# Performance work log

Measured on AMD Instinct MI355X. Metric: run time of the kernel, lower is better.

## Reference

```python
import jax, jax.numpy as jnp
import numpy as np

E = 1024
H = 16
D = E // H  # 64
S = 2048
B = 4


def setup_inputs() -> dict:
    key = jax.random.key(0)
    ks = jax.random.split(key, 9)
    scale = 1.0 / np.sqrt(E)
    inp = {"x": jax.random.normal(ks[0], (S, B, E), dtype=jnp.float32)}
    for i, name in enumerate(["q", "k", "v", "o"]):
        inp[f"W{name}"] = jax.random.uniform(ks[1 + 2 * i], (E, E), dtype=jnp.float32, minval=-scale, maxval=scale)
        inp[f"b{name}"] = jax.random.uniform(ks[2 + 2 * i], (E,), dtype=jnp.float32, minval=-scale, maxval=scale)
    return inp


def reference(x, Wq, bq, Wk, bk, Wv, bv, Wo, bo):
    s, b, e = x.shape
    # linear projections (torch Linear: x @ W.T + b), split into heads
    q = (x @ Wq.T + bq).reshape(s, b, H, D)
    k = (x @ Wk.T + bk).reshape(s, b, H, D)
    v = (x @ Wv.T + bv).reshape(s, b, H, D)
    # naive O(S^2) attention, scores: [S, B, H, S]
    scores = jnp.einsum('sbhd,tbhd->sbht', q, k) / np.sqrt(D).astype(np.float32)
    attn = jax.nn.softmax(scores, axis=3)
    # dropout p=0.0 (eval) -> identity
    out = jnp.einsum('sbht,tbhd->sbhd', attn, v).reshape(s, b, e)
    return out @ Wo.T + bo
```

## Files before the change

### kernel.cpp

```cpp
#include <hip/hip_runtime.h>
#include <hip/hip_bf16.h>

#define S_LEN 2048
#define BATCH 4
#define EMB   1024
#define NH    16
#define HD    64
#define NROW  8192

#define QSCALE 0.18033688011112043f

typedef __bf16 bf16x8 __attribute__((ext_vector_type(8)));
typedef float  f32x4  __attribute__((ext_vector_type(4)));

typedef __attribute__((address_space(3))) void lds_void;
typedef const __attribute__((address_space(1))) void gbl_void;
#define GLOAD_LDS16(g, l) __builtin_amdgcn_global_load_lds((gbl_void*)(g), (lds_void*)(l), 16, 0, 0)
#define MFMA16(a, b, c) __builtin_amdgcn_mfma_f32_16x16x32_bf16((a), (b), (c), 0, 0, 0)

#if __has_builtin(__builtin_amdgcn_exp2f)
#define EXP2(x) __builtin_amdgcn_exp2f(x)
#else
#define EXP2(x) __expf((x) * 0.6931471805599453f)
#endif

__global__ void cvt_all_kernel(const float* __restrict__ x,
                               const float* __restrict__ wq, const float* __restrict__ wk,
                               const float* __restrict__ wv, const float* __restrict__ wo,
                               __bf16* __restrict__ xb,
                               __bf16* __restrict__ qb, __bf16* __restrict__ kb,
                               __bf16* __restrict__ vb, __bf16* __restrict__ ob) {
    const int bid = blockIdx.x;
    const float* src;
    __bf16* dst;
    int i;
    if (bid < 8192) {
        src = x; dst = xb; i = bid * 256 + threadIdx.x;
    } else {
        const int w = (bid - 8192) >> 10;
        src = w == 0 ? wq : (w == 1 ? wk : (w == 2 ? wv : wo));
        dst = w == 0 ? qb : (w == 1 ? kb : (w == 2 ? vb : ob));
        i = ((bid - 8192) & 1023) * 256 + threadIdx.x;
    }
    float4 v = ((const float4*)src)[i];
    union { __bf16 h[4]; short4 s4; } u;
    u.h[0] = (__bf16)v.x; u.h[1] = (__bf16)v.y;
    u.h[2] = (__bf16)v.z; u.h[3] = (__bf16)v.w;
    ((short4*)dst)[i] = u.s4;
}

__global__ __launch_bounds__(256) void gemm_qkv_kernel(
    const __bf16* __restrict__ A,
    const __bf16* __restrict__ W0, const __bf16* __restrict__ W1,
    const __bf16* __restrict__ W2,
    const float* __restrict__ bi0, const float* __restrict__ bi1,
    const float* __restrict__ bi2,
    __bf16* __restrict__ Qo, __bf16* __restrict__ Ko, __bf16* __restrict__ Vo)
{
    __shared__ __align__(16) char SMEM[49152];
    __bf16* Asb = (__bf16*)SMEM;
    __bf16* Bsb = (__bf16*)(SMEM + 24576);

    const int flat = blockIdx.x;
    const int xcd = flat & 7, slot = flat >> 3;
    const int nB = slot >> 3;
    const int mB = (xcd << 3) | (slot & 7);
    const int which = nB >> 3;
    const __bf16* W = which == 0 ? W0 : (which == 1 ? W1 : W2);
    const float* bias = which == 0 ? bi0 : (which == 1 ? bi1 : bi2);
    __bf16* outb = which == 0 ? Qo : (which == 1 ? Ko : Vo);
    const int m0 = mB * 128;
    const int n0 = (nB & 7) * 128;

    const int lane = threadIdx.x & 63;
    const int wave = threadIdx.x >> 6;
    const int l15 = lane & 15;
    const int quad = lane >> 4;
    const int wm = (wave >> 1) * 64;
    const int wn = (wave & 1) * 64;

    const int c0 = wave * 128 + lane;
    const int c1 = c0 + 64;
    const int ar0 = c0 >> 2, ak0 = (((c0 & 3) ^ ((c0 >> 3) & 3))) * 8;
    const int ar1 = c1 >> 2, ak1 = (((c1 & 3) ^ ((c1 >> 3) & 3))) * 8;

    const __bf16* Ag = A + (size_t)m0 * EMB;
    const __bf16* Wg = W + (size_t)n0 * EMB;

    f32x4 acc[4][4];
#pragma unroll
    for (int i = 0; i < 4; ++i)
#pragma unroll
        for (int j = 0; j < 4; ++j) acc[i][j] = (f32x4){0.f, 0.f, 0.f, 0.f};

    auto stage = [&](int t, int buf) {
        const int kk = t * 32;
        GLOAD_LDS16(Ag + (size_t)ar0 * EMB + kk + ak0, Asb + buf * 4096 + wave * 1024);
        GLOAD_LDS16(Ag + (size_t)ar1 * EMB + kk + ak1, Asb + buf * 4096 + wave * 1024 + 512);
        GLOAD_LDS16(Wg + (size_t)ar0 * EMB + kk + ak0, Bsb + buf * 4096 + wave * 1024);
        GLOAD_LDS16(Wg + (size_t)ar1 * EMB + kk + ak1, Bsb + buf * 4096 + wave * 1024 + 512);
    };
    stage(0, 0);
    stage(1, 1);

    const int xr = (l15 >> 1) & 3;
    int bt = 0;
    for (int t = 0; t < 32; ++t) {
        if (t < 31) asm volatile("s_waitcnt vmcnt(4)" ::: "memory");
        else        asm volatile("s_waitcnt vmcnt(0)" ::: "memory");
        __builtin_amdgcn_s_barrier();
        if (t + 2 < 32) {
            int wb = bt + 2; if (wb >= 3) wb -= 3;
            stage(t + 2, wb);
        }
        bf16x8 af[4], bfr[4];
#pragma unroll
        for (int tt = 0; tt < 4; ++tt) {
            af[tt]  = *(const bf16x8*)(Asb + bt * 4096 + (wm + tt * 16 + l15) * 32 + ((quad ^ xr) << 3));
            bfr[tt] = *(const bf16x8*)(Bsb + bt * 4096 + (wn + tt * 16 + l15) * 32 + ((quad ^ xr) << 3));
        }
#pragma unroll
        for (int i = 0; i < 4; ++i)
#pragma unroll
            for (int j = 0; j < 4; ++j)
                acc[i][j] = MFMA16(af[i], bfr[j], acc[i][j]);
        if (++bt == 3) bt = 0;
    }

    __syncthreads();
    __bf16* epi = (__bf16*)SMEM + wave * 2304;
    float bv[4];
#pragma unroll
    for (int j = 0; j < 4; ++j) bv[j] = bias[n0 + wn + j * 16 + l15];
    const int hh = (n0 + wn) >> 6;

    if (which != 2) {
#pragma unroll
        for (int p = 0; p < 2; ++p) {
#pragma unroll
            for (int ih = 0; ih < 2; ++ih) {
                const int i = 2 * p + ih;
#pragma unroll
                for (int j = 0; j < 4; ++j)
#pragma unroll
                    for (int r = 0; r < 4; ++r) {
                        float v = acc[i][j][r] + bv[j];
                        if (which == 0) v *= QSCALE;
                        epi[(ih * 16 + quad * 4 + r) * 72 + j * 16 + l15] = (__bf16)v;
                    }
            }
#pragma unroll
            for (int ii = 0; ii < 4; ++ii) {
                const int rl = ii * 8 + (lane >> 3);
                bf16x8 row = *(const bf16x8*)(epi + rl * 72 + (lane & 7) * 8);
                const int m = m0 + wm + p * 32 + rl;
                const int b = m & 3, s = m >> 2;
                *(bf16x8*)(outb + ((size_t)(b * NH + hh) * S_LEN + s) * HD
                           + (lane & 7) * 8) = row;
            }
        }
    } else {
        const int sb = (m0 + wm) >> 2;
#pragma unroll
        for (int p = 0; p < 2; ++p) {
#pragma unroll
            for (int jh = 0; jh < 2; ++jh) {
                const int j = 2 * p + jh;
#pragma unroll
                for (int i = 0; i < 4; ++i)
#pragma unroll
                    for (int r = 0; r < 4; ++r) {
                        float v = acc[i][j][r] + bv[j];
                        epi[(jh * 16 + l15) * 72 + r * 16 + i * 4 + quad] = (__bf16)v;
                    }
            }
#pragma unroll
            for (int ii = 0; ii < 4; ++ii) {
                const int q = lane >> 1;
                bf16x8 row = *(const bf16x8*)(epi + q * 72 + ii * 16 + (lane & 1) * 8);
                const int d = p * 32 + q;
                *(bf16x8*)(outb + ((size_t)(ii * NH + hh) * HD + d) * S_LEN
                           + sb + (lane & 1) * 8) = row;
            }
        }
    }
}

__global__ __launch_bounds__(256) void gemm_out_kernel(
    const __bf16* __restrict__ A, const __bf16* __restrict__ W,
    const float* __restrict__ bias, float* __restrict__ outf)
{
    __shared__ __bf16 As[3][128 * 32];
    __shared__ __bf16 Bs[3][128 * 32];
    const int flat = blockIdx.x;
    const int xcd = flat & 7, slot = flat >> 3;
    const int nB = slot >> 3;
    const int mB = (xcd << 3) | (slot & 7);
    const int m0 = mB * 128;
    const int n0 = nB * 128;

    const int lane = threadIdx.x & 63;
    const int wave = threadIdx.x >> 6;
    const int l15 = lane & 15;
    const int quad = lane >> 4;
    const int wm = (wave >> 1) * 64;
    const int wn = (wave & 1) * 64;

    const int c0 = wave * 128 + lane;
    const int c1 = c0 + 64;
    const int ar0 = c0 >> 2, ak0 = (((c0 & 3) ^ ((c0 >> 3) & 3))) * 8;
    const int ar1 = c1 >> 2, ak1 = (((c1 & 3) ^ ((c1 >> 3) & 3))) * 8;

    const __bf16* Ag = A + (size_t)m0 * EMB;
    const __bf16* Wg = W + (size_t)n0 * EMB;

    f32x4 acc[4][4];
#pragma unroll
    for (int i = 0; i < 4; ++i)
#pragma unroll
        for (int j = 0; j < 4; ++j) acc[i][j] = (f32x4){0.f, 0.f, 0.f, 0.f};

    auto stage = [&](int t, int buf) {
        const int kk = t * 32;
        GLOAD_LDS16(Ag + (size_t)ar0 * EMB + kk + ak0, &As[buf][wave * 1024]);
        GLOAD_LDS16(Ag + (size_t)ar1 * EMB + kk + ak1, &As[buf][wave * 1024 + 512]);
        GLOAD_LDS16(Wg + (size_t)ar0 * EMB + kk + ak0, &Bs[buf][wave * 1024]);
        GLOAD_LDS16(Wg + (size_t)ar1 * EMB + kk + ak1, &Bs[buf][wave * 1024 + 512]);
    };
    stage(0, 0);
    stage(1, 1);

    const int xr = (l15 >> 1) & 3;
    int bt = 0;
    for (int t = 0; t < 32; ++t) {
        if (t < 31) asm volatile("s_waitcnt vmcnt(4)" ::: "memory");
        else        asm volatile("s_waitcnt vmcnt(0)" ::: "memory");
        __builtin_amdgcn_s_barrier();
        if (t + 2 < 32) {
            int wb = bt + 2; if (wb >= 3) wb -= 3;
            stage(t + 2, wb);
        }
        bf16x8 af[4], bfr[4];
#pragma unroll
        for (int tt = 0; tt < 4; ++tt) {
            af[tt]  = *(const bf16x8*)(&As[bt][0] + (wm + tt * 16 + l15) * 32 + ((quad ^ xr) << 3));
            bfr[tt] = *(const bf16x8*)(&Bs[bt][0] + (wn + tt * 16 + l15) * 32 + ((quad ^ xr) << 3));
        }
#pragma unroll
        for (int i = 0; i < 4; ++i)
#pragma unroll
            for (int j = 0; j < 4; ++j)
                acc[i][j] = MFMA16(af[i], bfr[j], acc[i][j]);
        if (++bt == 3) bt = 0;
    }

#pragma unroll
    for (int j = 0; j < 4; ++j) {
        const int col = n0 + wn + j * 16 + l15;
        const float bv = bias[col];
#pragma unroll
        for (int i = 0; i < 4; ++i)
#pragma unroll
            for (int r = 0; r < 4; ++r) {
                const int m = m0 + wm + i * 16 + quad * 4 + r;
                outf[(size_t)m * EMB + col] = acc[i][j][r] + bv;
            }
    }
}

__global__ __launch_bounds__(256, 4) void attn_kernel(
    const __bf16* __restrict__ Q, const __bf16* __restrict__ Kp,
    const __bf16* __restrict__ Vt, __bf16* __restrict__ Ao)
{
    __shared__ __align__(16) __bf16 Ks[3][32 * 64];
    __shared__ __align__(16) __bf16 Vs[3][32 * 64];
    __shared__ __align__(16) __bf16 Ps[4][32 * 40];

    const int tid = threadIdx.x;
    const int lane = tid & 63;
    const int wave = tid >> 6;
    const int l15 = lane & 15;
    const int quad = lane >> 4;

    const int flat = blockIdx.y * gridDim.x + blockIdx.x;
    const int nf = (flat & 7) * 128 + (flat >> 3);
    const int bh = nf >> 4;
    const int b = bh >> 4, h = bh & 15;
    const int qw = (nf & 15) * 128 + wave * 32;

    const __bf16* Qb = Q  + (size_t)bh * S_LEN * HD;
    const __bf16* Kb = Kp + (size_t)bh * S_LEN * HD;
    const __bf16* Vb = Vt + (size_t)bh * HD * S_LEN;

    const int kr = tid >> 3;
    const int ks = (((tid & 7) ^ ((tid >> 4) & 7))) * 8;
    const int vr = tid >> 2;
    const int vs = (((tid & 3) ^ ((tid >> 3) & 3))) * 8;

    bf16x8 qf[2][2];
#pragma unroll
    for (int mi = 0; mi < 2; ++mi)
#pragma unroll
        for (int kc = 0; kc < 2; ++kc)
            qf[mi][kc] = *(const bf16x8*)(Qb + (size_t)(qw + mi * 16 + l15) * HD
                                          + kc * 32 + quad * 8);

    bf16x8 ones;
#pragma unroll
    for (int i = 0; i < 8; ++i) ones[i] = (__bf16)1.0f;

    f32x4 acco[2][4], accl[2];
#pragma unroll
    for (int mi = 0; mi < 2; ++mi) {
        accl[mi] = (f32x4){0.f, 0.f, 0.f, 0.f};
#pragma unroll
        for (int nt = 0; nt < 4; ++nt) acco[mi][nt] = (f32x4){0.f, 0.f, 0.f, 0.f};
    }

    auto stageKV = [&](int t, int buf) {
        const int t0 = t * 32;
        GLOAD_LDS16(Kb + (size_t)(t0 + kr) * HD + ks, &Ks[buf][wave * 512]);
        GLOAD_LDS16(Vb + (size_t)vr * S_LEN + t0 + vs, &Vs[buf][wave * 512]);
    };
    stageKV(0, 0);
    stageKV(1, 1);

    int bt = 0;
    for (int it = 0; it < S_LEN / 32; ++it) {
        if (it < S_LEN / 32 - 1) asm volatile("s_waitcnt vmcnt(2)" ::: "memory");
        else                     asm volatile("s_waitcnt vmcnt(0)" ::: "memory");
        __builtin_amdgcn_s_barrier();
        if (it + 2 < S_LEN / 32) {
            int wb = bt + 2; if (wb >= 3) wb -= 3;
            stageKV(it + 2, wb);
        }
        const __bf16* Kt = &Ks[bt][0];
        const __bf16* Vl = &Vs[bt][0];
        __bf16* Pw = &Ps[wave][0];

        bf16x8 kf[2][2];
#pragma unroll
        for (int p = 0; p < 2; ++p) {
            const int r = 2 * l15 + p;
            const int x = l15 & 7;
#pragma unroll
            for (int kc = 0; kc < 2; ++kc)
                kf[p][kc] = *(const bf16x8*)(Kt + r * 64 + (((kc * 4 + quad) ^ x) << 3));
        }
#pragma unroll
        for (int mi = 0; mi < 2; ++mi) {
            f32x4 se = {0.f, 0.f, 0.f, 0.f}, so = {0.f, 0.f, 0.f, 0.f};
            se = MFMA16(qf[mi][0], kf[0][0], se);
            se = MFMA16(qf[mi][1], kf[0][1], se);
            so = MFMA16(qf[mi][0], kf[1][0], so);
            so = MFMA16(qf[mi][1], kf[1][1], so);
#pragma unroll
            for (int r = 0; r < 4; ++r) {
                float pe = EXP2(se[r]);
                float po = EXP2(so[r]);
                union { __bf16 hh[2]; unsigned u; } pk;
                pk.hh[0] = (__bf16)pe;
                pk.hh[1] = (__bf16)po;
                *(unsigned*)(Pw + (mi * 16 + quad * 4 + r) * 40 + 2 * l15) = pk.u;
            }
        }
        bf16x8 pf[2];
#pragma unroll
        for (int mi = 0; mi < 2; ++mi) {
            pf[mi] = *(const bf16x8*)(Pw + (mi * 16 + l15) * 40 + quad * 8);
            accl[mi] = MFMA16(pf[mi], ones, accl[mi]);
        }
#pragma unroll
        for (int nt = 0; nt < 4; ++nt) {
            const int rv = nt * 16 + l15;
            const int xv = (l15 >> 1) & 3;
            bf16x8 vf = *(const bf16x8*)(Vl + rv * 32 + (((quad ^ xv)) << 3));
#pragma unroll
            for (int mi = 0; mi < 2; ++mi)
                acco[mi][nt] = MFMA16(pf[mi], vf, acco[mi][nt]);
        }
        if (++bt == 3) bt = 0;
    }

#pragma unroll
    for (int mi = 0; mi < 2; ++mi)
#pragma unroll
        for (int r = 0; r < 4; ++r) {
            const float inv = 1.0f / accl[mi][r];
            const int srow = qw + mi * 16 + quad * 4 + r;
            const int n = srow * BATCH + b;
#pragma unroll
            for (int nt = 0; nt < 4; ++nt)
                Ao[(size_t)n * EMB + h * 64 + nt * 16 + l15] =
                    (__bf16)(acco[mi][nt][r] * inv);
        }
}

extern "C" void kernel_launch(void* const* d_in, const int* in_sizes, int n_in,
                              void* d_out, int out_size, void* d_ws, size_t ws_size,
                              hipStream_t stream) {
    const float* x  = (const float*)d_in[0];
    const float* Wq = (const float*)d_in[1];
    const float* bq = (const float*)d_in[2];
    const float* Wk = (const float*)d_in[3];
    const float* bk = (const float*)d_in[4];
    const float* Wv = (const float*)d_in[5];
    const float* bv = (const float*)d_in[6];
    const float* Wo = (const float*)d_in[7];
    const float* bo = (const float*)d_in[8];
    float* out = (float*)d_out;

    char* ws = (char*)d_ws;
    const size_t xbf_sz = (size_t)NROW * EMB * 2;
    const size_t wbf_sz = (size_t)EMB * EMB * 2;
    const size_t qkv_sz = (size_t)BATCH * NH * S_LEN * HD * 2;
    __bf16* x_bf  = (__bf16*)ws;  ws += xbf_sz;
    __bf16* Wq_bf = (__bf16*)ws;  ws += wbf_sz;
    __bf16* Wk_bf = (__bf16*)ws;  ws += wbf_sz;
    __bf16* Wv_bf = (__bf16*)ws;  ws += wbf_sz;
    __bf16* Wo_bf = (__bf16*)ws;  ws += wbf_sz;
    __bf16* Qb    = (__bf16*)ws;  ws += qkv_sz;
    __bf16* Kb    = (__bf16*)ws;  ws += qkv_sz;
    __bf16* Vtb   = (__bf16*)ws;  ws += qkv_sz;
    __bf16* Aob   = (__bf16*)ws;  ws += qkv_sz;

    cvt_all_kernel<<<8192 + 4 * 1024, 256, 0, stream>>>(
        x, Wq, Wk, Wv, Wo, x_bf, Wq_bf, Wk_bf, Wv_bf, Wo_bf);

    gemm_qkv_kernel<<<64 * 24, 256, 0, stream>>>(x_bf, Wq_bf, Wk_bf, Wv_bf,
                                                 bq, bk, bv, Qb, Kb, Vtb);
    dim3 ag(S_LEN / 128, BATCH * NH);
    attn_kernel<<<ag, 256, 0, stream>>>(Qb, Kb, Vtb, Aob);
    gemm_out_kernel<<<(NROW / 128) * (EMB / 128), 256, 0, stream>>>(Aob, Wo_bf, bo, out);
}
```

Baseline: 277.1 us.

## Software-pipeline attention loop: overlap PV of previous tile with QK/exp of current

Restructures the attention inner loop so each iteration runs the P·V MFMAs for the previous key tile before the QK^T and exp2 for the current tile. The P scratch is double-buffered per wave and V gets a fourth LDS buffer so its tile stays live one iteration longer. The goal is to let MFMA work overlap the exp/transcendental and LDS round-trip latency of the softmax stage. In exchange it uses more LDS, and launch bounds drop from 4 to 3 blocks per CU, which lowers occupancy.

```diff
diff --git a/kernel.cpp b/kernel.cpp
--- a/kernel.cpp
+++ b/kernel.cpp
@@ -268,13 +268,13 @@
     }
 }
 
-__global__ __launch_bounds__(256, 4) void attn_kernel(
+__global__ __launch_bounds__(256, 3) void attn_kernel(
     const __bf16* __restrict__ Q, const __bf16* __restrict__ Kp,
     const __bf16* __restrict__ Vt, __bf16* __restrict__ Ao)
 {
     __shared__ __align__(16) __bf16 Ks[3][32 * 64];
-    __shared__ __align__(16) __bf16 Vs[3][32 * 64];
-    __shared__ __align__(16) __bf16 Ps[4][32 * 40];
+    __shared__ __align__(16) __bf16 Vs[4][32 * 64];
+    __shared__ __align__(16) __bf16 Ps[4][2][32 * 40];
 
     const int tid = threadIdx.x;
     const int lane = tid & 63;
@@ -317,27 +317,15 @@
         for (int nt = 0; nt < 4; ++nt) acco[mi][nt] = (f32x4){0.f, 0.f, 0.f, 0.f};
     }
 
-    auto stageKV = [&](int t, int buf) {
+    auto stageKV = [&](int t) {
         const int t0 = t * 32;
-        GLOAD_LDS16(Kb + (size_t)(t0 + kr) * HD + ks, &Ks[buf][wave * 512]);
-        GLOAD_LDS16(Vb + (size_t)vr * S_LEN + t0 + vs, &Vs[buf][wave * 512]);
+        GLOAD_LDS16(Kb + (size_t)(t0 + kr) * HD + ks, &Ks[t % 3][wave * 512]);
+        GLOAD_LDS16(Vb + (size_t)vr * S_LEN + t0 + vs, &Vs[t & 3][wave * 512]);
     };
-    stageKV(0, 0);
-    stageKV(1, 1);
-
-    int bt = 0;
-    for (int it = 0; it < S_LEN / 32; ++it) {
-        if (it < S_LEN / 32 - 1) asm volatile("s_waitcnt vmcnt(2)" ::: "memory");
-        else                     asm volatile("s_waitcnt vmcnt(0)" ::: "memory");
-        __builtin_amdgcn_s_barrier();
-        if (it + 2 < S_LEN / 32) {
-            int wb = bt + 2; if (wb >= 3) wb -= 3;
-            stageKV(it + 2, wb);
-        }
-        const __bf16* Kt = &Ks[bt][0];
-        const __bf16* Vl = &Vs[bt][0];
-        __bf16* Pw = &Ps[wave][0];
-
+
+    auto qk_exp = [&](int it) {
+        const __bf16* Kt = &Ks[it % 3][0];
+        __bf16* Pw = &Ps[wave][it & 1][0];
         bf16x8 kf[2][2];
 #pragma unroll
         for (int p = 0; p < 2; ++p) {
@@ -364,6 +352,11 @@
                 *(unsigned*)(Pw + (mi * 16 + quad * 4 + r) * 40 + 2 * l15) = pk.u;
             }
         }
+    };
+
+    auto pv = [&](int it) {
+        const __bf16* Vl = &Vs[it & 3][0];
+        const __bf16* Pw = &Ps[wave][it & 1][0];
         bf16x8 pf[2];
 #pragma unroll
         for (int mi = 0; mi < 2; ++mi) {
@@ -379,8 +372,25 @@
             for (int mi = 0; mi < 2; ++mi)
                 acco[mi][nt] = MFMA16(pf[mi], vf, acco[mi][nt]);
         }
-        if (++bt == 3) bt = 0;
-    }
+    };
+
+    stageKV(0);
+    stageKV(1);
+
+    asm volatile("s_waitcnt vmcnt(2)" ::: "memory");
+    __builtin_amdgcn_s_barrier();
+    stageKV(2);
+    qk_exp(0);
+
+    for (int it = 1; it < S_LEN / 32; ++it) {
+        if (it < S_LEN / 32 - 1) asm volatile("s_waitcnt vmcnt(2)" ::: "memory");
+        else                     asm volatile("s_waitcnt vmcnt(0)" ::: "memory");
+        __builtin_amdgcn_s_barrier();
+        if (it + 2 < S_LEN / 32) stageKV(it + 2);
+        pv(it - 1);
+        qk_exp(it);
+    }
+    pv(S_LEN / 32 - 1);
 
 #pragma unroll
     for (int mi = 0; mi < 2; ++mi)
```

Measured after the change: 288.9 us. 4.3% more time.

## Compute transposed scores to keep P in registers, dropping LDS round-trip

Applied to the files above, without the earlier changes.

The attention kernel now computes S^T (K as the A operand, Q as B) with a permuted key-row mapping, so each lane's MFMA output already forms the bf16x8 A-operand fragment for the P·V MFMA. This removes the per-wave P scratch buffer in LDS along with its stores and reloads. The K staging swizzle is changed to match the new row access pattern. Buffer indexing now uses it%3 instead of a rotating counter.

```diff
diff --git a/kernel.cpp b/kernel.cpp
--- a/kernel.cpp
+++ b/kernel.cpp
@@ -274,7 +274,6 @@
 {
     __shared__ __align__(16) __bf16 Ks[3][32 * 64];
     __shared__ __align__(16) __bf16 Vs[3][32 * 64];
-    __shared__ __align__(16) __bf16 Ps[4][32 * 40];
 
     const int tid = threadIdx.x;
     const int lane = tid & 63;
@@ -293,7 +292,7 @@
     const __bf16* Vb = Vt + (size_t)bh * HD * S_LEN;
 
     const int kr = tid >> 3;
-    const int ks = (((tid & 7) ^ ((tid >> 4) & 7))) * 8;
+    const int ks = ((tid & 7) ^ ((kr & 3) | (((kr >> 3) & 1) << 2))) * 8;
     const int vr = tid >> 2;
     const int vs = (((tid & 3) ^ ((tid >> 3) & 3))) * 8;
 
@@ -317,69 +316,58 @@
         for (int nt = 0; nt < 4; ++nt) acco[mi][nt] = (f32x4){0.f, 0.f, 0.f, 0.f};
     }
 
-    auto stageKV = [&](int t, int buf) {
+    auto stageKV = [&](int t) {
         const int t0 = t * 32;
-        GLOAD_LDS16(Kb + (size_t)(t0 + kr) * HD + ks, &Ks[buf][wave * 512]);
-        GLOAD_LDS16(Vb + (size_t)vr * S_LEN + t0 + vs, &Vs[buf][wave * 512]);
+        GLOAD_LDS16(Kb + (size_t)(t0 + kr) * HD + ks, &Ks[t % 3][wave * 512]);
+        GLOAD_LDS16(Vb + (size_t)vr * S_LEN + t0 + vs, &Vs[t % 3][wave * 512]);
     };
-    stageKV(0, 0);
-    stageKV(1, 1);
-
-    int bt = 0;
+    stageKV(0);
+    stageKV(1);
+
+    const int ta = 8 * (l15 >> 2) + (l15 & 3);
+    const int xk = (l15 & 3) | (((l15 >> 2) & 1) << 2);
+    const int xv = (l15 >> 1) & 3;
+
     for (int it = 0; it < S_LEN / 32; ++it) {
         if (it < S_LEN / 32 - 1) asm volatile("s_waitcnt vmcnt(2)" ::: "memory");
         else                     asm volatile("s_waitcnt vmcnt(0)" ::: "memory");
         __builtin_amdgcn_s_barrier();
-        if (it + 2 < S_LEN / 32) {
-            int wb = bt + 2; if (wb >= 3) wb -= 3;
-            stageKV(it + 2, wb);
-        }
-        const __bf16* Kt = &Ks[bt][0];
-        const __bf16* Vl = &Vs[bt][0];
-        __bf16* Pw = &Ps[wave][0];
-
-        bf16x8 kf[2][2];
-#pragma unroll
-        for (int p = 0; p < 2; ++p) {
-            const int r = 2 * l15 + p;
-            const int x = l15 & 7;
-#pragma unroll
-            for (int kc = 0; kc < 2; ++kc)
-                kf[p][kc] = *(const bf16x8*)(Kt + r * 64 + (((kc * 4 + quad) ^ x) << 3));
-        }
+        if (it + 2 < S_LEN / 32) stageKV(it + 2);
+
+        const __bf16* Kt = &Ks[it % 3][0];
+        const __bf16* Vl = &Vs[it % 3][0];
+
+        bf16x8 kfA[2], kfB[2];
+#pragma unroll
+        for (int kc = 0; kc < 2; ++kc) {
+            kfA[kc] = *(const bf16x8*)(Kt + ta * 64 + (((kc * 4 + quad) ^ xk) << 3));
+            kfB[kc] = *(const bf16x8*)(Kt + (ta + 4) * 64 + (((kc * 4 + quad) ^ xk) << 3));
+        }
+        bf16x8 pf[2];
 #pragma unroll
         for (int mi = 0; mi < 2; ++mi) {
-            f32x4 se = {0.f, 0.f, 0.f, 0.f}, so = {0.f, 0.f, 0.f, 0.f};
-            se = MFMA16(qf[mi][0], kf[0][0], se);
-            se = MFMA16(qf[mi][1], kf[0][1], se);
-            so = MFMA16(qf[mi][0], kf[1][0], so);
-            so = MFMA16(qf[mi][1], kf[1][1], so);
+            f32x4 sA = {0.f, 0.f, 0.f, 0.f}, sB = {0.f, 0.f, 0.f, 0.f};
+            sA = MFMA16(kfA[0], qf[mi][0], sA);
+            sA = MFMA16(kfA[1], qf[mi][1], sA);
+            sB = MFMA16(kfB[0], qf[mi][0], sB);
+            sB = MFMA16(kfB[1], qf[mi][1], sB);
+            union { __bf16 hh[8]; bf16x8 v; } u;
 #pragma unroll
             for (int r = 0; r < 4; ++r) {
-                float pe = EXP2(se[r]);
-                float po = EXP2(so[r]);
-                union { __bf16 hh[2]; unsigned u; } pk;
-                pk.hh[0] = (__bf16)pe;
-                pk.hh[1] = (__bf16)po;
-                *(unsigned*)(Pw + (mi * 16 + quad * 4 + r) * 40 + 2 * l15) = pk.u;
-            }
-        }
-        bf16x8 pf[2];
-#pragma unroll
-        for (int mi = 0; mi < 2; ++mi) {
-            pf[mi] = *(const bf16x8*)(Pw + (mi * 16 + l15) * 40 + quad * 8);
+                u.hh[r]     = (__bf16)EXP2(sA[r]);
+                u.hh[4 + r] = (__bf16)EXP2(sB[r]);
+            }
+            pf[mi] = u.v;
             accl[mi] = MFMA16(pf[mi], ones, accl[mi]);
         }
 #pragma unroll
         for (int nt = 0; nt < 4; ++nt) {
             const int rv = nt * 16 + l15;
-            const int xv = (l15 >> 1) & 3;
-            bf16x8 vf = *(const bf16x8*)(Vl + rv * 32 + (((quad ^ xv)) << 3));
+            bf16x8 vf = *(const bf16x8*)(Vl + rv * 32 + ((quad ^ xv) << 3));
 #pragma unroll
             for (int mi = 0; mi < 2; ++mi)
                 acco[mi][nt] = MFMA16(pf[mi], vf, acco[mi][nt]);
         }
-        if (++bt == 3) bt = 0;
     }
 
 #pragma unroll
```

Measured after the change: 272.6 us. About the same (-1.6%).
